# Kernel tuning notes

Measured on AMD Instinct MI355X. Metric: run time of the kernel, lower is better.

The kernel has to match this reference:

```python
import jax, jax.numpy as jnp
import numpy as np

N = 100000
E = 1600000
IN_DIM, HID, OUT = 512, 256, 32
EPS = 1e-16  # matches PyG softmax denominator epsilon


def gat_layer(xp, a_src, a_dst, src, dst, n_nodes):
    """Single-head GAT propagate with sigmoid + segment softmax, scatter-add.
    xp: [N, C] projected features; a_src/a_dst: [N] per-node attention logits;
    src/dst: [E] edge endpoints (message flows src -> dst)."""
    alpha = jax.nn.sigmoid(a_src[src] + a_dst[dst])  # [E]
    m = jax.ops.segment_max(alpha, dst, num_segments=n_nodes)  # [N]
    ex = jnp.exp(alpha - m[dst])
    denom = jax.ops.segment_sum(ex, dst, num_segments=n_nodes)  # [N]
    a = ex / (denom[dst] + EPS)  # [E]
    msg = xp[src] * a[:, None]  # [E, C]
    return jax.ops.segment_sum(msg, dst, num_segments=n_nodes)  # [N, C]


def setup_inputs() -> dict:
    key = jax.random.key(0)
    k1, k2, k3, k4, k5, k6, k7, k8 = jax.random.split(key, 8)
    features = jax.random.normal(k1, (N, IN_DIM), dtype=jnp.float32)
    edge_index = jax.random.randint(k2, (2, E), 0, N, dtype=jnp.int64)
    g = 1.414
    W1 = jax.random.normal(k3, (IN_DIM, HID), dtype=jnp.float32) * (g * np.sqrt(2.0 / (IN_DIM + HID)))
    W2 = jax.random.normal(k4, (HID, OUT), dtype=jnp.float32) * (g * np.sqrt(2.0 / (HID + OUT)))
    att_src1 = jax.random.normal(k5, (HID,), dtype=jnp.float32) * (g * np.sqrt(2.0 / (1 + HID)))
    att_dst1 = jax.random.normal(k6, (HID,), dtype=jnp.float32) * (g * np.sqrt(2.0 / (1 + HID)))
    return {"features": features, "edge_index": edge_index, "W1": W1, "W2": W2,
            "att_src1": att_src1, "att_dst1": att_dst1}


def reference(features, edge_index, W1, W2, att_src1, att_dst1):
    src, dst = edge_index[0], edge_index[1]
    # conv1 (with attention)
    xp1 = features @ W1  # [N, HID]
    a_src = xp1 @ att_src1  # [N]
    a_dst = xp1 @ att_dst1  # [N]
    h1 = jax.nn.elu(gat_layer(xp1, a_src, a_dst, src, dst, N))
    # conv2 (attention=False -> plain linear, mean over 1 head)
    h2 = h1 @ W2  # [N, OUT]
    # conv3: weights tied to W2^T, attention tied to conv1's per-node logits
    xp3 = h2 @ W2.T  # [N, HID]
    h3 = jax.nn.elu(gat_layer(xp3, a_src, a_dst, src, dst, N))
    # conv4 (attention=False): weights tied to W1^T
    h4 = h3 @ W1.T  # [N, IN_DIM]
    return h2, h4
```

## Files before the change

kernel.cpp:

```cpp
#include <hip/hip_runtime.h>
#include <cstdint>
#include <cstddef>

#define INDIM 512
#define HIDD  256
#define OUTD  32
#define PCH   4096
#define SHIFT 9
#define SLABN 512

typedef __attribute__((ext_vector_type(4))) float f32x4;
typedef __attribute__((ext_vector_type(8))) short bf16x8;

static inline __device__ float b2f(unsigned short u) {
  union { float f; unsigned int i; } v; v.i = ((unsigned int)u) << 16; return v.f;
}
static inline __device__ unsigned short f2b(float f) {
  union { float f; unsigned int i; } v; v.f = f;
  unsigned int x = v.i;
  x += 0x7fffu + ((x >> 16) & 1u);
  return (unsigned short)(x >> 16);
}

static inline __device__ float edgew(float x) {
  float al = 1.f / (1.f + __expf(-x));
  return __expf(al);
}

static __device__ __forceinline__ void gld16(const unsigned short* g, unsigned short* l) {
  __builtin_amdgcn_global_load_lds(
      (const __attribute__((address_space(1))) void*)g,
      (__attribute__((address_space(3))) void*)l, 16, 0, 0);
}

__global__ __launch_bounds__(256) void probe_kernel(
    const unsigned int* __restrict__ feat, const unsigned int* __restrict__ eidx,
    int* __restrict__ flags)
{
  int t = threadIdx.x;
  __shared__ int cnt, oddnz;
  if (t == 0) { cnt = 0; oddnz = 0; }
  __syncthreads();
  unsigned int w = feat[t];
  unsigned short lo = (unsigned short)(w & 0xFFFFu);
  int e = (lo >> 7) & 0xFF;
  int plausible = ((lo & 0x7FFF) == 0) || (e >= 0x60 && e <= 0x9F);
  atomicAdd(&cnt, plausible);
  if (t & 1) { if (eidx[t] != 0u) atomicAdd(&oddnz, 1); }
  __syncthreads();
  if (t == 0) { flags[0] = (cnt >= 192) ? 1 : 0; flags[1] = (oddnz == 0) ? 1 : 0; }
}

__global__ __launch_bounds__(256) void cnt_kernel(
    const unsigned int* __restrict__ eidx, int* __restrict__ bcnt,
    int E, const int* __restrict__ flags)
{
  __shared__ int hist[256];
  int t = threadIdx.x;
  hist[t] = 0;
  __syncthreads();
  int e0 = blockIdx.x * PCH;
  const int i64 = flags[1];
  for (int i = t; i < PCH; i += 256) {
    int e = e0 + i; if (e >= E) break;
    int d = i64 ? (int)eidx[2 * ((size_t)E + e)] : (int)eidx[(size_t)E + e];
    atomicAdd(&hist[d >> SHIFT], 1);
  }
  __syncthreads();
  bcnt[blockIdx.x * 256 + t] = hist[t];
}

__global__ __launch_bounds__(256) void bscan_kernel(
    int* __restrict__ bcnt, int* __restrict__ slabOff, int npb)
{
  __shared__ int wsum[4];
  int t = threadIdx.x, lane = t & 63, wv = t >> 6;
  int run = 0;
  for (int b = 0; b < npb; ++b) {
    int v = bcnt[b * 256 + t];
    bcnt[b * 256 + t] = run;
    run += v;
  }
  int inc = run;
#pragma unroll
  for (int o = 1; o < 64; o <<= 1) {
    int u = __shfl_up(inc, o);
    if (lane >= o) inc += u;
  }
  if (lane == 63) wsum[wv] = inc;
  __syncthreads();
  if (t < 4) {
    int v = wsum[t], s = v;
#pragma unroll
    for (int o = 1; o < 4; o <<= 1) {
      int u = __shfl_up(s, o);
      if (t >= o) s += u;
    }
    wsum[t] = s - v;
  }
  __syncthreads();
  int exc = wsum[wv] + inc - run;
  slabOff[t] = exc;
  if (t == 255) slabOff[256] = exc + run;
}

__global__ __launch_bounds__(256) void scat_kernel(
    const unsigned int* __restrict__ eidx, const int* __restrict__ bcnt,
    const int* __restrict__ slabOff, uint2* __restrict__ part,
    int E, const int* __restrict__ flags)
{
  __shared__ int cur[256];
  int t = threadIdx.x;
  cur[t] = slabOff[t] + bcnt[blockIdx.x * 256 + t];
  __syncthreads();
  int e0 = blockIdx.x * PCH;
  const int i64 = flags[1];
  for (int i = t; i < PCH; i += 256) {
    int e = e0 + i; if (e >= E) break;
    int s, d;
    if (i64) { s = (int)eidx[2 * (size_t)e]; d = (int)eidx[2 * ((size_t)E + e)]; }
    else     { s = (int)eidx[e];             d = (int)eidx[(size_t)E + e]; }
    int pos = atomicAdd(&cur[d >> SHIFT], 1);
    part[pos] = make_uint2((unsigned)s, (unsigned)d);
  }
}

__global__ __launch_bounds__(256) void slabcsr_kernel(
    const uint2* __restrict__ part, const int* __restrict__ slabOff,
    int* __restrict__ offs, int* __restrict__ srcP, int N, int nslab)
{
  __shared__ int deg[SLABN];
  __shared__ int wsum[4];
  int sl = blockIdx.x, t = threadIdx.x;
  int n0 = sl << SHIFT;
  int nn = N - n0; if (nn > SLABN) nn = SLABN;
  int s0 = slabOff[sl], s1 = slabOff[sl + 1];
  for (int i = t; i < SLABN; i += 256) deg[i] = 0;
  __syncthreads();
  for (int i = s0 + t; i < s1; i += 256)
    atomicAdd(&deg[(int)part[i].y - n0], 1);
  __syncthreads();
  int bi = t * 2;
  int l0 = deg[bi], l1 = deg[bi + 1];
  int s = l0 + l1;
  int ws = s;
#pragma unroll
  for (int o = 1; o < 64; o <<= 1) {
    int u = __shfl_up(ws, o);
    if ((t & 63) >= o) ws += u;
  }
  if ((t & 63) == 63) wsum[t >> 6] = ws;
  __syncthreads();
  if (t < 4) {
    int v = wsum[t], inc = v;
#pragma unroll
    for (int o = 1; o < 4; o <<= 1) {
      int u = __shfl_up(inc, o);
      if (t >= o) inc += u;
    }
    wsum[t] = inc - v;
  }
  __syncthreads();
  int run = wsum[t >> 6] + (ws - s);
  deg[bi] = run;
  if (bi < nn) offs[n0 + bi] = s0 + run;
  run += l0;
  deg[bi + 1] = run;
  if (bi + 1 < nn) offs[n0 + bi + 1] = s0 + run;
  __syncthreads();
  for (int i = s0 + t; i < s1; i += 256) {
    uint2 p = part[i];
    int pos = s0 + atomicAdd(&deg[(int)p.y - n0], 1);
    srcP[pos] = (int)p.x;
  }
  if (sl == nslab - 1 && t == 0) offs[N] = s1;
}

static inline __device__ float ldadapt(const void* p, size_t i, int isbf) {
  return isbf ? b2f(((const unsigned short*)p)[i]) : ((const float*)p)[i];
}

__global__ __launch_bounds__(256) void prep_weights(
    const void* __restrict__ W1, const void* __restrict__ W2,
    const void* __restrict__ aS, const void* __restrict__ aD,
    unsigned short* __restrict__ W1b, unsigned short* __restrict__ W1tb,
    float* __restrict__ W2f, unsigned short* __restrict__ W2b64,
    float* __restrict__ atS, float* __restrict__ atD,
    const int* __restrict__ flags)
{
  const int fb = flags[0];
  int i = blockIdx.x * 256 + threadIdx.x;
  if (i < INDIM * HIDD) {
    int r = i >> 8, c = i & 255;
    float w0 = ldadapt(W1, i, fb);
    unsigned short wb = f2b(w0);
    W1b[i] = wb;
    W1tb[c * INDIM + r] = wb;
  }
  if (i < HIDD * OUTD) {
    int r = i >> 5, c = i & 31;
    float w0 = ldadapt(W2, i, fb);
    W2f[i] = w0;
    W2b64[r * 64 + c] = f2b(w0);
    W2b64[r * 64 + 32 + c] = 0;
  }
  if (i < HIDD) { atS[i] = ldadapt(aS, i, fb); atD[i] = ldadapt(aD, i, fb); }
}

template<int AMODE, int OUTMODE, int EPI>
__global__ __launch_bounds__(256) void gemm_nt2(
    const void* __restrict__ Av, const unsigned short* __restrict__ Bt,
    unsigned short* __restrict__ Cb, void* __restrict__ Out, size_t outOff,
    const int* __restrict__ flags, int M, int Nn, int K)
{
  __shared__ unsigned short Als[128 * 64];
  __shared__ unsigned short Bls[128 * 64];
  const int tid = threadIdx.x, lane = tid & 63, wid = tid >> 6;
  const int wr = wid >> 1, wc = wid & 1;
  const int rowBase = blockIdx.y * 128, colBase = blockIdx.x * 128;
  const int fb = flags[0];

  const int srow = (lane >> 3), sg = lane & 7;
  const int sgx = sg ^ srow;

  f32x4 acc[4][4] = {};

  for (int kt = 0; kt < K; kt += 64) {
    if (AMODE == 1 && !fb) {
      const float* Af = (const float*)Av;
#pragma unroll
      for (int i = 0; i < 4; ++i) {
        int row = wid * 32 + i * 8 + srow;
        int gr = rowBase + row; if (gr > M - 1) gr = M - 1;
        const float* sp = Af + (size_t)gr * K + kt + sg * 8;
        float4 lo = *(const float4*)sp;
        float4 hi = *(const float4*)(sp + 4);
        union { unsigned short us[8]; int4 v; } cv;
        cv.us[0] = f2b(lo.x); cv.us[1] = f2b(lo.y); cv.us[2] = f2b(lo.z); cv.us[3] = f2b(lo.w);
        cv.us[4] = f2b(hi.x); cv.us[5] = f2b(hi.y); cv.us[6] = f2b(hi.z); cv.us[7] = f2b(hi.w);
        *(int4*)(Als + (wid * 4 + i) * 512 + srow * 64 + (sgx << 3)) = cv.v;
      }
    } else {
      const unsigned short* Ab = (const unsigned short*)Av;
#pragma unroll
      for (int i = 0; i < 4; ++i) {
        int row = wid * 32 + i * 8 + srow;
        int gr = rowBase + row;
        if (AMODE == 1 && gr > M - 1) gr = M - 1;
        gld16(Ab + (size_t)gr * K + kt + (sgx << 3), Als + (wid * 4 + i) * 512);
      }
    }
#pragma unroll
    for (int i = 0; i < 4; ++i) {
      int row = wid * 32 + i * 8 + srow;
      gld16(Bt + (size_t)(colBase + row) * K + kt + (sgx << 3), Bls + (wid * 4 + i) * 512);
    }
    __syncthreads();

    bf16x8 af[4], bfr[4];
#pragma unroll
    for (int ks = 0; ks < 2; ++ks) {
      int gl = ks * 4 + (lane >> 4);
      int gx = gl ^ (lane & 7);
#pragma unroll
      for (int mi = 0; mi < 4; ++mi) {
        int row = wr * 64 + mi * 16 + (lane & 15);
        af[mi] = *(const bf16x8*)(Als + row * 64 + (gx << 3));
      }
#pragma unroll
      for (int ni = 0; ni < 4; ++ni) {
        int row = wc * 64 + ni * 16 + (lane & 15);
        bfr[ni] = *(const bf16x8*)(Bls + row * 64 + (gx << 3));
      }
#pragma unroll
      for (int mi = 0; mi < 4; ++mi)
#pragma unroll
        for (int ni = 0; ni < 4; ++ni)
          acc[mi][ni] = __builtin_amdgcn_mfma_f32_16x16x32_bf16(af[mi], bfr[ni], acc[mi][ni], 0, 0, 0);
    }
    __syncthreads();
  }

#pragma unroll
  for (int mi = 0; mi < 4; ++mi) {
    int r0 = rowBase + wr * 64 + mi * 16 + (lane >> 4) * 4;
#pragma unroll
    for (int ni = 0; ni < 4; ++ni) {
      int c = colBase + wc * 64 + ni * 16 + (lane & 15);
#pragma unroll
      for (int v = 0; v < 4; ++v) {
        int r = r0 + v;
        if (r < M) {
          size_t idx = (size_t)r * Nn + c;
          float x = acc[mi][ni][v];
          if (EPI) x = x > 0.f ? x : expm1f(x);
          if (OUTMODE == 0) Cb[idx] = f2b(x);
          else {
            if (fb) ((unsigned short*)Out)[outOff + idx] = f2b(x);
            else    ((float*)Out)[outOff + idx] = x;
          }
        }
      }
    }
  }
}

__global__ __launch_bounds__(256) void rowdots(
    const unsigned short* __restrict__ P, const float* __restrict__ atS,
    const float* __restrict__ atD,
    float* __restrict__ asrc, float* __restrict__ adst, int N)
{
  int wave = threadIdx.x >> 6, lane = threadIdx.x & 63;
  int node = blockIdx.x * 4 + wave;
  if (node >= N) return;
  ushort4 u = *(const ushort4*)(P + (size_t)node * HIDD + lane * 4);
  float4 v = make_float4(b2f(u.x), b2f(u.y), b2f(u.z), b2f(u.w));
  float4 s = *(const float4*)(atS + lane * 4);
  float4 d = *(const float4*)(atD + lane * 4);
  float s1 = v.x * s.x + v.y * s.y + v.z * s.z + v.w * s.w;
  float s2 = v.x * d.x + v.y * d.y + v.z * d.z + v.w * d.w;
#pragma unroll
  for (int off = 32; off; off >>= 1) {
    s1 += __shfl_down(s1, off);
    s2 += __shfl_down(s2, off);
  }
  if (lane == 0) { asrc[node] = s1; adst[node] = s2; }
}

__global__ __launch_bounds__(256) void agg_elu2(
    const unsigned short* __restrict__ xp,
    const float* __restrict__ asrc, const float* __restrict__ adst,
    const int* __restrict__ srcP, const int* __restrict__ offs,
    unsigned short* __restrict__ hout, int N)
{
  __shared__ int   sS[4][64];
  __shared__ float sW[4][64];
  int wid = threadIdx.x >> 6, lane = threadIdx.x & 63;
  int node = blockIdx.x * 4 + wid;
  if (node >= N) return;
  const float ad = adst[node];
  int s0 = offs[node], s1 = offs[node + 1];
  float a0 = 0.f, a1 = 0.f, a2 = 0.f, a3 = 0.f, den = 0.f;
  for (int base = s0; base < s1; base += 64) {
    int cnt = s1 - base; if (cnt > 64) cnt = 64;
    if (lane < cnt) {
      int sv = srcP[base + lane];
      sS[wid][lane] = sv;
      sW[wid][lane] = edgew(asrc[sv] + ad);
    }
    asm volatile("s_waitcnt lgkmcnt(0)" ::: "memory");
    int j = 0;
    for (; j + 16 <= cnt; j += 16) {
      ushort4 u[16];
#pragma unroll
      for (int q = 0; q < 16; ++q)
        u[q] = *(const ushort4*)(xp + (size_t)sS[wid][j + q] * HIDD + lane * 4);
#pragma unroll
      for (int q = 0; q < 16; ++q) {
        float wv = sW[wid][j + q];
        den += wv;
        a0 += wv * b2f(u[q].x); a1 += wv * b2f(u[q].y);
        a2 += wv * b2f(u[q].z); a3 += wv * b2f(u[q].w);
      }
    }
    for (; j + 8 <= cnt; j += 8) {
      ushort4 u[8];
#pragma unroll
      for (int q = 0; q < 8; ++q)
        u[q] = *(const ushort4*)(xp + (size_t)sS[wid][j + q] * HIDD + lane * 4);
#pragma unroll
      for (int q = 0; q < 8; ++q) {
        float wv = sW[wid][j + q];
        den += wv;
        a0 += wv * b2f(u[q].x); a1 += wv * b2f(u[q].y);
        a2 += wv * b2f(u[q].z); a3 += wv * b2f(u[q].w);
      }
    }
    for (; j < cnt; ++j) {
      int   sv = sS[wid][j];
      float wv = sW[wid][j];
      den += wv;
      ushort4 u = *(const ushort4*)(xp + (size_t)sv * HIDD + lane * 4);
      a0 += wv * b2f(u.x); a1 += wv * b2f(u.y); a2 += wv * b2f(u.z); a3 += wv * b2f(u.w);
    }
  }
  float inv = 1.f / (den + 1e-16f);
  float r0 = a0 * inv, r1 = a1 * inv, r2 = a2 * inv, r3 = a3 * inv;
  r0 = r0 > 0.f ? r0 : expm1f(r0);
  r1 = r1 > 0.f ? r1 : expm1f(r1);
  r2 = r2 > 0.f ? r2 : expm1f(r2);
  r3 = r3 > 0.f ? r3 : expm1f(r3);
  ushort4 o; o.x = f2b(r0); o.y = f2b(r1); o.z = f2b(r2); o.w = f2b(r3);
  *(ushort4*)(hout + (size_t)node * HIDD + lane * 4) = o;
}

__global__ __launch_bounds__(256) void gemm_h2(
    const unsigned short* __restrict__ H1, const float* __restrict__ W2f,
    void* __restrict__ Out, unsigned short* __restrict__ h2b,
    const int* __restrict__ flags, int M)
{
  const int fb = flags[0];
  __shared__ float Bs[HIDD][33];
  __shared__ float As[8][HIDD];
  int tid = threadIdx.x;
  int tx = tid & 31, ty = tid >> 5;
  int row0 = blockIdx.x * 8;
#pragma unroll
  for (int j = 0; j < 8; ++j) {
    int idx4 = tid + 256 * j;
    float4 v = *(const float4*)(W2f + idx4 * 4);
    int k = idx4 >> 3, c = (idx4 & 7) * 4;
    Bs[k][c] = v.x; Bs[k][c + 1] = v.y; Bs[k][c + 2] = v.z; Bs[k][c + 3] = v.w;
  }
  {
    int flat = tid * 8;
    int r = flat >> 8, k = flat & 255;
    int gr = row0 + r;
    if (gr < M) {
      ushort4 lo = *(const ushort4*)(H1 + (size_t)gr * HIDD + k);
      ushort4 hi = *(const ushort4*)(H1 + (size_t)gr * HIDD + k + 4);
      As[r][k] = b2f(lo.x); As[r][k + 1] = b2f(lo.y); As[r][k + 2] = b2f(lo.z); As[r][k + 3] = b2f(lo.w);
      As[r][k + 4] = b2f(hi.x); As[r][k + 5] = b2f(hi.y); As[r][k + 6] = b2f(hi.z); As[r][k + 7] = b2f(hi.w);
    } else {
#pragma unroll
      for (int q = 0; q < 8; ++q) As[r][k + q] = 0.f;
    }
  }
  __syncthreads();
  float acc = 0.f;
#pragma unroll 8
  for (int k = 0; k < HIDD; ++k) acc += As[ty][k] * Bs[k][tx];
  int row = row0 + ty;
  if (row < M) {
    size_t idx = (size_t)row * OUTD + tx;
    if (fb) ((unsigned short*)Out)[idx] = f2b(acc);
    else    ((float*)Out)[idx] = acc;
    h2b[idx] = f2b(acc);
  }
}

__global__ __launch_bounds__(256) void agg_small(
    const unsigned short* __restrict__ h2b,
    const float* __restrict__ asrc, const float* __restrict__ adst,
    const int* __restrict__ srcP, const int* __restrict__ offs,
    unsigned short* __restrict__ g2pad, int N)
{
  int wid = threadIdx.x >> 6, lane = threadIdx.x & 63;
  int node = blockIdx.x * 4 + wid;
  if (node >= N) return;
  int grp = lane >> 4, cl = lane & 15;
  const float ad = adst[node];
  int s0 = offs[node], s1 = offs[node + 1];
  float a0 = 0.f, a1 = 0.f, den = 0.f;
  for (int e = s0 + grp; e < s1; e += 4) {
    int   sv = srcP[e];
    float wv = edgew(asrc[sv] + ad);
    den += wv;
    ushort2 u = *(const ushort2*)(h2b + (size_t)sv * OUTD + cl * 2);
    a0 += wv * b2f(u.x);
    a1 += wv * b2f(u.y);
  }
  a0 += __shfl_xor(a0, 16); a0 += __shfl_xor(a0, 32);
  a1 += __shfl_xor(a1, 16); a1 += __shfl_xor(a1, 32);
  den += __shfl_xor(den, 16); den += __shfl_xor(den, 32);
  if (grp == 0) {
    float inv = 1.f / (den + 1e-16f);
    ushort2 o; o.x = f2b(a0 * inv); o.y = f2b(a1 * inv);
    *(ushort2*)(g2pad + (size_t)node * 64 + cl * 2) = o;
  } else if (grp == 1) {
    *(ushort2*)(g2pad + (size_t)node * 64 + 32 + cl * 2) = make_ushort2(0, 0);
  }
}

extern "C" void kernel_launch(void* const* d_in, const int* in_sizes, int n_in,
                              void* d_out, int out_size, void* d_ws, size_t ws_size,
                              hipStream_t stream)
{
  const void*         feat = d_in[0];
  const unsigned int* eidx = (const unsigned int*)d_in[1];
  const void*         W1   = d_in[2];
  const void*         W2   = d_in[3];
  const void*         aS   = d_in[4];
  const void*         aD   = d_in[5];

  const int N = in_sizes[0] / INDIM;
  const int E = in_sizes[1] / 2;
  const int M_pad = ((N + 127) / 128) * 128;
  const int nslab = (N + SLABN - 1) / SLABN;
  const int npb = (E + PCH - 1) / PCH;

  char* w = (char*)d_ws;
  auto alloc = [&](size_t bytes) -> char* {
    char* p = w; w += (bytes + 255) & ~(size_t)255; return p;
  };
  unsigned short* H     = (unsigned short*)alloc((size_t)M_pad * HIDD * 2);
  unsigned short* P     = (unsigned short*)alloc((size_t)M_pad * HIDD * 2);
  unsigned short* h2b   = (unsigned short*)alloc((size_t)N * OUTD * 2);
  unsigned short* g2pad = (unsigned short*)alloc((size_t)M_pad * 64 * 2);
  float* asrc = (float*)alloc((size_t)N * 4);
  float* adst = (float*)alloc((size_t)N * 4);
  int*   srcP = (int*)alloc((size_t)E * 4);
  uint2* part = (uint2*)alloc((size_t)E * 8);
  int*   offs = (int*)alloc((size_t)(N + 1) * 4);
  int*   bcnt = (int*)alloc((size_t)npb * 256 * 4);
  int*   slabOff = (int*)alloc(257 * 4);
  unsigned short* W1b   = (unsigned short*)alloc((size_t)INDIM * HIDD * 2);
  unsigned short* W1tb  = (unsigned short*)alloc((size_t)INDIM * HIDD * 2);
  unsigned short* W2b64 = (unsigned short*)alloc((size_t)HIDD * 64 * 2);
  float* W2f  = (float*)alloc((size_t)HIDD * OUTD * 4);
  float* atS  = (float*)alloc((size_t)HIDD * 4);
  float* atD  = (float*)alloc((size_t)HIDD * 4);
  int*   flags = (int*)alloc(64);

  probe_kernel<<<1, 256, 0, stream>>>((const unsigned int*)feat, eidx, flags);

  cnt_kernel<<<npb, 256, 0, stream>>>(eidx, bcnt, E, flags);
  bscan_kernel<<<1, 256, 0, stream>>>(bcnt, slabOff, npb);
  scat_kernel<<<npb, 256, 0, stream>>>(eidx, bcnt, slabOff, part, E, flags);
  slabcsr_kernel<<<nslab, 256, 0, stream>>>(part, slabOff, offs, srcP, N, nslab);

  prep_weights<<<512, 256, 0, stream>>>(W1, W2, aS, aD, W1b, W1tb, W2f, W2b64, atS, atD, flags);

  const int mb = (N + 127) / 128;

  gemm_nt2<1, 0, 0><<<dim3(HIDD / 128, mb), 256, 0, stream>>>(
      feat, W1tb, P, nullptr, 0, flags, N, HIDD, INDIM);

  rowdots<<<(N + 3) / 4, 256, 0, stream>>>(P, atS, atD, asrc, adst, N);

  agg_elu2<<<(N + 3) / 4, 256, 0, stream>>>(P, asrc, adst, srcP, offs, H, N);

  gemm_h2<<<(N + 7) / 8, 256, 0, stream>>>(H, W2f, d_out, h2b, flags, N);

  agg_small<<<(N + 3) / 4, 256, 0, stream>>>(h2b, asrc, adst, srcP, offs, g2pad, N);

  gemm_nt2<0, 0, 1><<<dim3(HIDD / 128, mb), 256, 0, stream>>>(
      g2pad, W2b64, H, nullptr, 0, flags, N, HIDD, 64);

  gemm_nt2<0, 1, 0><<<dim3(INDIM / 128, mb), 256, 0, stream>>>(
      H, W1b, nullptr, d_out, (size_t)N * OUTD, flags, N, INDIM, HIDD);
}
```

Measured before the change: 657.9 us.

## Double-buffer LDS tiles in bf16 GEMM to overlap loads with MFMA

Shared-memory A and B tiles become double buffers, so the next K-tile is loaded while the current one is computed. The fp32 A path prefetches into registers and converts and writes to LDS after compute, and the loop drops one barrier per iteration. The aim is to hide global load latency behind the MFMA work. In exchange, LDS use doubles to 64KB per block, which may lower occupancy, and the fp32 register prefetch raises register pressure.

```diff
diff --git a/kernel.cpp b/kernel.cpp
--- a/kernel.cpp
+++ b/kernel.cpp
@@ -213,8 +213,8 @@
     unsigned short* __restrict__ Cb, void* __restrict__ Out, size_t outOff,
     const int* __restrict__ flags, int M, int Nn, int K)
 {
-  __shared__ unsigned short Als[128 * 64];
-  __shared__ unsigned short Bls[128 * 64];
+  __shared__ unsigned short Als[2][128 * 64];
+  __shared__ unsigned short Bls[2][128 * 64];
   const int tid = threadIdx.x, lane = tid & 63, wid = tid >> 6;
   const int wr = wid >> 1, wc = wid & 1;
   const int rowBase = blockIdx.y * 128, colBase = blockIdx.x * 128;
@@ -224,39 +224,48 @@
   const int sgx = sg ^ srow;
 
   f32x4 acc[4][4] = {};
-
-  for (int kt = 0; kt < K; kt += 64) {
-    if (AMODE == 1 && !fb) {
-      const float* Af = (const float*)Av;
-#pragma unroll
-      for (int i = 0; i < 4; ++i) {
-        int row = wid * 32 + i * 8 + srow;
-        int gr = rowBase + row; if (gr > M - 1) gr = M - 1;
-        const float* sp = Af + (size_t)gr * K + kt + sg * 8;
-        float4 lo = *(const float4*)sp;
-        float4 hi = *(const float4*)(sp + 4);
-        union { unsigned short us[8]; int4 v; } cv;
-        cv.us[0] = f2b(lo.x); cv.us[1] = f2b(lo.y); cv.us[2] = f2b(lo.z); cv.us[3] = f2b(lo.w);
-        cv.us[4] = f2b(hi.x); cv.us[5] = f2b(hi.y); cv.us[6] = f2b(hi.z); cv.us[7] = f2b(hi.w);
-        *(int4*)(Als + (wid * 4 + i) * 512 + srow * 64 + (sgx << 3)) = cv.v;
-      }
-    } else {
-      const unsigned short* Ab = (const unsigned short*)Av;
-#pragma unroll
-      for (int i = 0; i < 4; ++i) {
-        int row = wid * 32 + i * 8 + srow;
-        int gr = rowBase + row;
-        if (AMODE == 1 && gr > M - 1) gr = M - 1;
-        gld16(Ab + (size_t)gr * K + kt + (sgx << 3), Als + (wid * 4 + i) * 512);
-      }
-    }
+  const int nt = K / 64;
+
+  auto stageB16 = [&](int buf, int kt) {
 #pragma unroll
     for (int i = 0; i < 4; ++i) {
       int row = wid * 32 + i * 8 + srow;
-      gld16(Bt + (size_t)(colBase + row) * K + kt + (sgx << 3), Bls + (wid * 4 + i) * 512);
-    }
-    __syncthreads();
-
+      gld16(Bt + (size_t)(colBase + row) * K + kt + (sgx << 3), &Bls[buf][(wid * 4 + i) * 512]);
+    }
+  };
+  auto stageA16 = [&](int buf, int kt) {
+    const unsigned short* Ab = (const unsigned short*)Av;
+#pragma unroll
+    for (int i = 0; i < 4; ++i) {
+      int row = wid * 32 + i * 8 + srow;
+      int gr = rowBase + row;
+      if (AMODE == 1 && gr > M - 1) gr = M - 1;
+      gld16(Ab + (size_t)gr * K + kt + (sgx << 3), &Als[buf][(wid * 4 + i) * 512]);
+    }
+  };
+  float4 pf[8];
+  auto loadAf32 = [&](int kt) {
+    const float* Af = (const float*)Av;
+#pragma unroll
+    for (int i = 0; i < 4; ++i) {
+      int row = wid * 32 + i * 8 + srow;
+      int gr = rowBase + row; if (gr > M - 1) gr = M - 1;
+      const float* sp = Af + (size_t)gr * K + kt + sg * 8;
+      pf[2 * i] = *(const float4*)sp;
+      pf[2 * i + 1] = *(const float4*)(sp + 4);
+    }
+  };
+  auto writeAf32 = [&](int buf) {
+#pragma unroll
+    for (int i = 0; i < 4; ++i) {
+      float4 lo = pf[2 * i], hi = pf[2 * i + 1];
+      union { unsigned short us[8]; int4 v; } cv;
+      cv.us[0] = f2b(lo.x); cv.us[1] = f2b(lo.y); cv.us[2] = f2b(lo.z); cv.us[3] = f2b(lo.w);
+      cv.us[4] = f2b(hi.x); cv.us[5] = f2b(hi.y); cv.us[6] = f2b(hi.z); cv.us[7] = f2b(hi.w);
+      *(int4*)(&Als[buf][(wid * 4 + i) * 512 + srow * 64 + (sgx << 3)]) = cv.v;
+    }
+  };
+  auto compute = [&](int buf) {
     bf16x8 af[4], bfr[4];
 #pragma unroll
     for (int ks = 0; ks < 2; ++ks) {
@@ -265,12 +274,12 @@
 #pragma unroll
       for (int mi = 0; mi < 4; ++mi) {
         int row = wr * 64 + mi * 16 + (lane & 15);
-        af[mi] = *(const bf16x8*)(Als + row * 64 + (gx << 3));
+        af[mi] = *(const bf16x8*)(&Als[buf][row * 64 + (gx << 3)]);
       }
 #pragma unroll
       for (int ni = 0; ni < 4; ++ni) {
         int row = wc * 64 + ni * 16 + (lane & 15);
-        bfr[ni] = *(const bf16x8*)(Bls + row * 64 + (gx << 3));
+        bfr[ni] = *(const bf16x8*)(&Bls[buf][row * 64 + (gx << 3)]);
       }
 #pragma unroll
       for (int mi = 0; mi < 4; ++mi)
@@ -278,7 +287,31 @@
         for (int ni = 0; ni < 4; ++ni)
           acc[mi][ni] = __builtin_amdgcn_mfma_f32_16x16x32_bf16(af[mi], bfr[ni], acc[mi][ni], 0, 0, 0);
     }
+  };
+
+  if (AMODE == 1 && !fb) {
+    loadAf32(0);
+    writeAf32(0);
+    stageB16(0, 0);
     __syncthreads();
+    int cur = 0;
+    for (int t = 0; t < nt; ++t) {
+      if (t + 1 < nt) { loadAf32((t + 1) * 64); stageB16(cur ^ 1, (t + 1) * 64); }
+      compute(cur);
+      if (t + 1 < nt) writeAf32(cur ^ 1);
+      __syncthreads();
+      cur ^= 1;
+    }
+  } else {
+    stageA16(0, 0); stageB16(0, 0);
+    __syncthreads();
+    int cur = 0;
+    for (int t = 0; t < nt; ++t) {
+      if (t + 1 < nt) { stageA16(cur ^ 1, (t + 1) * 64); stageB16(cur ^ 1, (t + 1) * 64); }
+      compute(cur);
+      __syncthreads();
+      cur ^= 1;
+    }
   }
 
 #pragma unroll
```

New measurement: 651.9 us. No clear change (-0.9%).
